# Kernel optimization log

Measured on AMD Instinct MI355X. Metric: run time of the kernel, lower is better.

## Reference

```python
import jax, jax.numpy as jnp
import numpy as np

S1, S2, B, H, E, IN, OUT, NL = 8, 32, 256, 1024, 512, 2, 2, 4


def setup_inputs() -> dict:
    key = jax.random.key(0)
    ks = jax.random.split(key, 20)
    s_h = 1.0 / np.sqrt(H)
    inp = {
        'input': jax.random.normal(ks[0], (B, IN), jnp.float32),
        'h0': jax.random.normal(ks[1], (NL, B, H), jnp.float32) * 0.5,
        'c0': jax.random.normal(ks[2], (NL, B, H), jnp.float32) * 0.5,
        'all_outputs': jax.random.normal(ks[3], (S1, S2, B, H), jnp.float32),
        'W_emb': jax.random.normal(ks[4], (E, IN), jnp.float32) / np.sqrt(IN),
        'b_emb': jax.random.normal(ks[5], (E,), jnp.float32) * 0.01,
        'W_attn': jax.random.normal(ks[6], (1, 2 * H), jnp.float32) / np.sqrt(2 * H),
        'b_attn': jax.random.normal(ks[7], (1,), jnp.float32) * 0.01,
        'Wih0': jax.random.normal(ks[8], (4 * H, E + H), jnp.float32) / np.sqrt(E + H),
        'Whh0': jax.random.normal(ks[9], (4 * H, H), jnp.float32) * s_h,
        'bih0': jax.random.normal(ks[10], (4 * H,), jnp.float32) * 0.01,
        'bhh0': jax.random.normal(ks[11], (4 * H,), jnp.float32) * 0.01,
        'Wih_r': jax.random.normal(ks[12], (NL - 1, 4 * H, H), jnp.float32) * s_h,
        'Whh_r': jax.random.normal(ks[13], (NL - 1, 4 * H, H), jnp.float32) * s_h,
        'bih_r': jax.random.normal(ks[14], (NL - 1, 4 * H), jnp.float32) * 0.01,
        'bhh_r': jax.random.normal(ks[15], (NL - 1, 4 * H), jnp.float32) * 0.01,
        'W_out': jax.random.normal(ks[16], (OUT, H), jnp.float32) * s_h,
        'b_out': jax.random.normal(ks[17], (OUT,), jnp.float32) * 0.01,
    }
    return inp


def _lstm_cell(x, h, c, Wih, Whh, bih, bhh):
    g = x @ Wih.T + h @ Whh.T + bih + bhh  # [B, 4H], torch gate order i,f,g,o
    i, f, gg, o = jnp.split(g, 4, axis=1)
    c2 = jax.nn.sigmoid(f) * c + jax.nn.sigmoid(i) * jnp.tanh(gg)
    h2 = jax.nn.sigmoid(o) * jnp.tanh(c2)
    return h2, c2


def reference(input, h0, c0, all_outputs, W_emb, b_emb, W_attn, b_attn,
              Wih0, Whh0, bih0, bhh0, Wih_r, Whh_r, bih_r, bhh_r, W_out, b_out):
    s1, s2, b, h_dim = all_outputs.shape
    # embedding (dropout = identity in eval mode)
    embedded = jax.nn.relu(input @ W_emb.T + b_emb)  # [B, E]
    h_top = h0[0]  # [B, H]
    # attn(cat(h_top, y)) decomposed: h part is shared across all (j, i)
    w_h = W_attn[0, :h_dim]
    w_y = W_attn[0, h_dim:]
    scores = (jnp.einsum('jibh,h->jib', all_outputs, w_y)
              + (h_top @ w_h)[None, None, :] + b_attn[0])  # [S1, S2, B]
    # torch cats per-(j,i) [B,1] columns j-major -> [B, S1*S2]
    normalized = jax.nn.softmax(scores.reshape(s1 * s2, b).T, axis=1)  # [B, S1*S2]
    temp = normalized.reshape(b, s1, s2)
    # NOTE: original writes into an expand()-ed zero buffer, so every j-slice
    # aliases the same memory; after the loop all slices equal the last j's bmm
    # result and sum(0) multiplies it by S1. We replicate that exactly.
    applied_last = jnp.einsum('bi,ibh->bh', temp[:, -1, :], all_outputs[-1])  # [B, H]
    final_attn = s1 * applied_last
    x = jnp.concatenate([final_attn, embedded], axis=1)  # [B, H+E]
    hs, cs = [], []
    h, c = _lstm_cell(x, h0[0], c0[0], Wih0, Whh0, bih0, bhh0)
    hs.append(h); cs.append(c)
    for l in range(Wih_r.shape[0]):  # inter-layer dropout = identity in eval
        h, c = _lstm_cell(h, h0[l + 1], c0[l + 1], Wih_r[l], Whh_r[l], bih_r[l], bhh_r[l])
        hs.append(h); cs.append(c)
    h_new = jnp.stack(hs)
    c_new = jnp.stack(cs)
    final_output = h @ W_out.T + b_out  # [B, OUT]
    return final_output, h_new, c_new, normalized
```

## Files before the change

### kernel.cpp

```cpp
#include <hip/hip_runtime.h>
#include <hip/hip_bf16.h>

typedef __bf16 bf16x8 __attribute__((ext_vector_type(8)));
typedef __bf16 bf16x4 __attribute__((ext_vector_type(4)));
typedef float  f32x4  __attribute__((ext_vector_type(4)));

#define KX 1536
#define G4 4096

#define O_FINAL 0
#define O_H     512
#define O_C     1049088
#define O_NORM  2097664

template<int K>
__device__ __forceinline__ void tile_gemm(const __bf16* __restrict__ A,
                                          const float* __restrict__ W,
                                          int r0, int j0,
                                          __bf16* __restrict__ At,
                                          __bf16* __restrict__ Wt,
                                          f32x4 acc[2]) {
  const int t = threadIdx.x;
  const int lane = t & 63, wave = t >> 6;
  const int rf = wave & 3, gg = wave >> 2;
  const int tr = t >> 3, chunk = t & 7;
  const int wrow = (tr >> 4) * 1024 + j0 + (tr & 15);
  const float*  wsrc = W + (size_t)wrow * K + chunk * 8;
  const __bf16* asrc = A + (size_t)(r0 + tr) * K + chunk * 8;
  const int sw_off = (chunk ^ (tr & 7)) << 4;
  char* wdst = (char*)Wt + tr * 128 + sw_off;
  char* adst = (char*)At + tr * 128 + sw_off;
  const int a_tr  = rf * 16 + (lane & 15);
  const int w_tr0 = gg * 32 + (lane & 15);
  const int w_tr1 = w_tr0 + 16;
  const int ksel  = lane >> 4;

  float4 wreg0 = *(const float4*)wsrc;
  float4 wreg1 = *(const float4*)(wsrc + 4);
  bf16x8 areg  = *(const bf16x8*)asrc;

  constexpr int NK = K / 64;
#pragma unroll 2
  for (int step = 0; step < NK; ++step) {
    __syncthreads();
    bf16x8 wv;
    wv[0] = (__bf16)wreg0.x; wv[1] = (__bf16)wreg0.y;
    wv[2] = (__bf16)wreg0.z; wv[3] = (__bf16)wreg0.w;
    wv[4] = (__bf16)wreg1.x; wv[5] = (__bf16)wreg1.y;
    wv[6] = (__bf16)wreg1.z; wv[7] = (__bf16)wreg1.w;
    *(bf16x8*)wdst = wv;
    *(bf16x8*)adst = areg;
    __syncthreads();
    if (step + 1 < NK) {
      wreg0 = *(const float4*)(wsrc + (step + 1) * 64);
      wreg1 = *(const float4*)(wsrc + (step + 1) * 64 + 4);
      areg  = *(const bf16x8*)(asrc + (step + 1) * 64);
    }
#pragma unroll
    for (int s = 0; s < 2; ++s) {
      const int chk = s * 4 + ksel;
      bf16x8 af  = *(const bf16x8*)((char*)At + a_tr  * 128 + ((chk ^ (a_tr  & 7)) << 4));
      bf16x8 wf0 = *(const bf16x8*)((char*)Wt + w_tr0 * 128 + ((chk ^ (w_tr0 & 7)) << 4));
      bf16x8 wf1 = *(const bf16x8*)((char*)Wt + w_tr1 * 128 + ((chk ^ (w_tr1 & 7)) << 4));
      acc[0] = __builtin_amdgcn_mfma_f32_16x16x32_bf16(af, wf0, acc[0], 0, 0, 0);
      acc[1] = __builtin_amdgcn_mfma_f32_16x16x32_bf16(af, wf1, acc[1], 0, 0, 0);
    }
  }
}

__global__ __launch_bounds__(256) void k_pre(const float* __restrict__ AO,
                                             const float* __restrict__ Wattn,
                                             const float* __restrict__ h0,
                                             float* __restrict__ sc,
                                             __bf16* __restrict__ h0b) {
  if (blockIdx.x >= 4096) {
    const int base = ((int)blockIdx.x - 4096) * 256 + threadIdx.x;
#pragma unroll
    for (int i = 0; i < 4; ++i) {
      int idx = base + i * 65536;
      float4 v = ((const float4*)h0)[idx];
      bf16x4 o;
      o[0] = (__bf16)v.x; o[1] = (__bf16)v.y; o[2] = (__bf16)v.z; o[3] = (__bf16)v.w;
      ((bf16x4*)h0b)[idx] = o;
    }
    return;
  }
  const int lane = threadIdx.x & 63, wave = threadIdx.x >> 6;
  const float* wy = Wattn + 1024;
  float4 wv[4];
#pragma unroll
  for (int q = 0; q < 4; ++q) wv[q] = *(const float4*)(wy + lane * 4 + 256 * q);
  const int row0 = (blockIdx.x * 4 + wave) * 4;
  float acc[4];
#pragma unroll
  for (int rr = 0; rr < 4; ++rr) {
    const float4* rp = (const float4*)(AO + (size_t)(row0 + rr) * 1024);
    float a = 0.f;
#pragma unroll
    for (int q = 0; q < 4; ++q) {
      float4 v = rp[lane + 64 * q];
      a += v.x * wv[q].x + v.y * wv[q].y + v.z * wv[q].z + v.w * wv[q].w;
    }
    acc[rr] = a;
  }
#pragma unroll
  for (int rr = 0; rr < 4; ++rr) {
    float a = acc[rr];
#pragma unroll
    for (int off = 32; off; off >>= 1) a += __shfl_xor(a, off, 64);
    if (lane == 0) {
      int row = row0 + rr;
      sc[(row & 255) * 256 + (row >> 8)] = a;
    }
  }
}

__global__ __launch_bounds__(512) void k_gh(const __bf16* __restrict__ h0b,
                                            const float* __restrict__ Whh0,
                                            const float* __restrict__ Whh_r,
                                            const float* __restrict__ bih0,
                                            const float* __restrict__ bhh0,
                                            const float* __restrict__ bih_r,
                                            const float* __restrict__ bhh_r,
                                            float* __restrict__ Gh) {
  __shared__ __bf16 At[64 * 64];
  __shared__ __bf16 Wt[64 * 64];
  const int l = blockIdx.x >> 8, inner = blockIdx.x & 255;
  const int cb = inner & 63, rb = inner >> 6;
  const int j0 = cb * 16, r0 = rb * 64;
  const __bf16* A = h0b + (size_t)l * 262144;
  const float* W  = (l == 0) ? Whh0 : (Whh_r + (size_t)(l - 1) * 4194304);
  const float* bi = (l == 0) ? bih0 : (bih_r + (size_t)(l - 1) * 4096);
  const float* bh = (l == 0) ? bhh0 : (bhh_r + (size_t)(l - 1) * 4096);
  f32x4 acc[2] = {};
  tile_gemm<1024>(A, W, r0, j0, At, Wt, acc);
  float* Go = Gh + (size_t)l * 1048576;
  const int lane = threadIdx.x & 63, wave = threadIdx.x >> 6;
  const int rf = wave & 3, gg = wave >> 2;
  const int col = j0 + (lane & 15);
  const int rbase = r0 + rf * 16 + ((lane >> 4) << 2);
#pragma unroll
  for (int gi = 0; gi < 2; ++gi) {
    const int cg = (gg * 2 + gi) * 1024 + col;
#pragma unroll
    for (int q = 0; q < 4; ++q)
      Go[(size_t)(rbase + q) * G4 + cg] = acc[gi][q] + bi[cg] + bh[cg];
  }
}

__global__ __launch_bounds__(256) void k_smx(const float* __restrict__ sc,
                                             const float* __restrict__ AO,
                                             const float* __restrict__ inp,
                                             const float* __restrict__ Wemb,
                                             const float* __restrict__ bemb,
                                             float* __restrict__ norm_out,
                                             __bf16* __restrict__ x) {
  __shared__ float red[4];
  __shared__ float wsm[32];
  const int b = blockIdx.x, t = threadIdx.x, lane = t & 63, wave = t >> 6;
  float s = sc[b * 256 + t];
  float m = s;
#pragma unroll
  for (int off = 32; off; off >>= 1) m = fmaxf(m, __shfl_xor(m, off, 64));
  if (lane == 0) red[wave] = m;
  __syncthreads();
  m = fmaxf(fmaxf(red[0], red[1]), fmaxf(red[2], red[3]));
  float e = __expf(s - m);
  float sum = e;
#pragma unroll
  for (int off = 32; off; off >>= 1) sum += __shfl_xor(sum, off, 64);
  __syncthreads();
  if (lane == 0) red[wave] = sum;
  __syncthreads();
  sum = red[0] + red[1] + red[2] + red[3];
  float nv = e / sum;
  norm_out[b * 256 + t] = nv;
  if (t >= 224) wsm[t - 224] = nv;
  __syncthreads();
  float acc[4] = {0.f, 0.f, 0.f, 0.f};
  const float* base = AO + ((size_t)224 * 256 + b) * 1024;
#pragma unroll 4
  for (int i = 0; i < 32; ++i) {
    float w = wsm[i];
    const float* rp = base + (size_t)i * 256 * 1024;
#pragma unroll
    for (int q = 0; q < 4; ++q) acc[q] += w * rp[t + 256 * q];
  }
#pragma unroll
  for (int q = 0; q < 4; ++q) x[(size_t)b * KX + t + 256 * q] = (__bf16)(8.0f * acc[q]);
  float i0 = inp[b * 2], i1 = inp[b * 2 + 1];
#pragma unroll
  for (int r = 0; r < 2; ++r) {
    int j = t + 256 * r;
    float e2 = i0 * Wemb[j * 2] + i1 * Wemb[j * 2 + 1] + bemb[j];
    x[(size_t)b * KX + 1024 + j] = (__bf16)fmaxf(e2, 0.f);
  }
}

template<int K>
__global__ __launch_bounds__(512) void k_layer(const __bf16* __restrict__ A,
                                               const float* __restrict__ Wih,
                                               const float* __restrict__ Gh,
                                               const float* __restrict__ c0,
                                               float* __restrict__ h_out,
                                               float* __restrict__ c_out,
                                               __bf16* __restrict__ hb) {
  __shared__ __bf16 At[64 * 64];
  __shared__ __bf16 Wt[64 * 64];
  __shared__ float exch[4][2][256];
  const int t = threadIdx.x, lane = t & 63, wave = t >> 6;
  const int rf = wave & 3, gg = wave >> 2;
  const int cb = blockIdx.x & 63, rb = blockIdx.x >> 6;
  const int j0 = cb * 16, r0 = rb * 64;
  f32x4 acc[2] = {};
  tile_gemm<K>(A, Wih, r0, j0, At, Wt, acc);
  const int col = j0 + (lane & 15);
  const int rbase = r0 + rf * 16 + ((lane >> 4) << 2);
#pragma unroll
  for (int gi = 0; gi < 2; ++gi) {
    const float* gp = Gh + (size_t)rbase * G4 + (gg * 2 + gi) * 1024 + col;
#pragma unroll
    for (int q = 0; q < 4; ++q) acc[gi][q] += gp[(size_t)q * G4];
  }
  const int eidx = ((lane >> 4) << 2) * 16 + (lane & 15);
  if (gg == 1) {
#pragma unroll
    for (int gi = 0; gi < 2; ++gi)
#pragma unroll
      for (int q = 0; q < 4; ++q)
        exch[rf][gi][eidx + q * 16] = acc[gi][q];
  }
  __syncthreads();
  if (gg == 0) {
#pragma unroll
    for (int q = 0; q < 4; ++q) {
      const int b = rbase + q;
      float gv = exch[rf][0][eidx + q * 16];
      float ov = exch[rf][1][eidx + q * 16];
      float si = 1.f / (1.f + __expf(-acc[0][q]));
      float sf = 1.f / (1.f + __expf(-acc[1][q]));
      float so = 1.f / (1.f + __expf(-ov));
      float c2 = sf * c0[(size_t)b * 1024 + col] + si * tanhf(gv);
      float h2 = so * tanhf(c2);
      h_out[(size_t)b * 1024 + col] = h2;
      c_out[(size_t)b * 1024 + col] = c2;
      hb[(size_t)b * 1024 + col] = (__bf16)h2;
    }
  }
}

__global__ __launch_bounds__(256) void k_final(const float* __restrict__ h3,
                                               const float* __restrict__ Wout,
                                               const float* __restrict__ bout,
                                               float* __restrict__ out) {
  const int lane = threadIdx.x & 63, wave = threadIdx.x >> 6;
  const int b = blockIdx.x * 4 + wave;
  const float4* hp = (const float4*)(h3 + (size_t)b * 1024);
  const float4* w0 = (const float4*)Wout;
  const float4* w1 = (const float4*)(Wout + 1024);
  float a0 = 0.f, a1 = 0.f;
#pragma unroll
  for (int q = 0; q < 4; ++q) {
    float4 hv = hp[lane + 64 * q];
    float4 v0 = w0[lane + 64 * q];
    float4 v1 = w1[lane + 64 * q];
    a0 += hv.x * v0.x + hv.y * v0.y + hv.z * v0.z + hv.w * v0.w;
    a1 += hv.x * v1.x + hv.y * v1.y + hv.z * v1.z + hv.w * v1.w;
  }
#pragma unroll
  for (int off = 32; off; off >>= 1) {
    a0 += __shfl_xor(a0, off, 64);
    a1 += __shfl_xor(a1, off, 64);
  }
  if (lane == 0) {
    out[b * 2]     = a0 + bout[0];
    out[b * 2 + 1] = a1 + bout[1];
  }
}

extern "C" void kernel_launch(void* const* d_in, const int* in_sizes, int n_in,
                              void* d_out, int out_size, void* d_ws, size_t ws_size,
                              hipStream_t stream) {
  const float* inp    = (const float*)d_in[0];
  const float* h0     = (const float*)d_in[1];
  const float* c0     = (const float*)d_in[2];
  const float* AO     = (const float*)d_in[3];
  const float* Wemb   = (const float*)d_in[4];
  const float* bemb   = (const float*)d_in[5];
  const float* Wattn  = (const float*)d_in[6];
  const float* Wih0   = (const float*)d_in[8];
  const float* Whh0   = (const float*)d_in[9];
  const float* bih0   = (const float*)d_in[10];
  const float* bhh0   = (const float*)d_in[11];
  const float* Wih_r  = (const float*)d_in[12];
  const float* Whh_r  = (const float*)d_in[13];
  const float* bih_r  = (const float*)d_in[14];
  const float* bhh_r  = (const float*)d_in[15];
  const float* Wout   = (const float*)d_in[16];
  const float* bout   = (const float*)d_in[17];

  float* out = (float*)d_out;
  char* ws = (char*)d_ws;

  float*  sc  = (float*)(ws + 0);
  float*  Gh  = (float*)(ws + (1u << 18));
  __bf16* xb  = (__bf16*)(ws + 17039360);
  __bf16* h0b = (__bf16*)(ws + 17825792);
  __bf16* hb  = (__bf16*)(ws + 19922944);

  k_pre<<<4352, 256, 0, stream>>>(AO, Wattn, h0, sc, h0b);
  k_gh<<<1024, 512, 0, stream>>>(h0b, Whh0, Whh_r, bih0, bhh0, bih_r, bhh_r, Gh);
  k_smx<<<256, 256, 0, stream>>>(sc, AO, inp, Wemb, bemb, out + O_NORM, xb);

  for (int l = 0; l < 4; ++l) {
    const __bf16* A1 = (l == 0) ? xb : (hb + (size_t)(l - 1) * 262144);
    float* h_out = out + O_H + (size_t)l * 262144;
    float* c_out = out + O_C + (size_t)l * 262144;
    if (l == 0)
      k_layer<1536><<<256, 512, 0, stream>>>(A1, Wih0, Gh, c0, h_out, c_out, hb);
    else
      k_layer<1024><<<256, 512, 0, stream>>>(A1, Wih_r + (size_t)(l - 1) * 4194304,
                                             Gh + (size_t)l * 1048576,
                                             c0 + (size_t)l * 262144,
                                             h_out, c_out,
                                             hb + (size_t)l * 262144);
  }

  k_final<<<64, 256, 0, stream>>>(out + O_H + 3 * 262144, Wout, bout, out + O_FINAL);
}
```

Baseline: 181.2 us.

## Fuse front kernels and precast input-gate weights to bf16 for layer GEMMs

Merges the attention-score, hidden-gate GEMM and a new weight-conversion pass into one wide front kernel. That kernel converts all Wih matrices to bf16 in parallel, so the four serial layer kernels stream half as many weight bytes. The Whh GEMM now reads fp32 h0 directly instead of a separate bf16 copy. The trade is extra total memory traffic (a bf16 weight write plus a reread) in exchange for a shorter serial critical path and one fewer launch.

```diff
diff --git a/kernel.cpp b/kernel.cpp
--- a/kernel.cpp
+++ b/kernel.cpp
@@ -4,28 +4,78 @@
 typedef __bf16 bf16x8 __attribute__((ext_vector_type(8)));
 typedef __bf16 bf16x4 __attribute__((ext_vector_type(4)));
 typedef float  f32x4  __attribute__((ext_vector_type(4)));
-
-#define KX 1536
-#define G4 4096
 
 #define O_FINAL 0
 #define O_H     512
 #define O_C     1049088
 #define O_NORM  2097664
 
+__device__ __forceinline__ bf16x8 cvt8(float4 a, float4 b) {
+  bf16x8 r;
+  r[0] = (__bf16)a.x; r[1] = (__bf16)a.y; r[2] = (__bf16)a.z; r[3] = (__bf16)a.w;
+  r[4] = (__bf16)b.x; r[5] = (__bf16)b.y; r[6] = (__bf16)b.z; r[7] = (__bf16)b.w;
+  return r;
+}
+
 template<int K>
-__device__ __forceinline__ void tile_gemm(const __bf16* __restrict__ A,
-                                          const float* __restrict__ W,
-                                          int r0, int j0,
-                                          __bf16* __restrict__ At,
-                                          __bf16* __restrict__ Wt,
-                                          f32x4 acc[2]) {
-  const int t = threadIdx.x;
-  const int lane = t & 63, wave = t >> 6;
+__device__ __forceinline__ void tile_gemm_ff(const float* __restrict__ A,
+                                             const float* __restrict__ W,
+                                             int r0, int j0,
+                                             __bf16* __restrict__ At,
+                                             __bf16* __restrict__ Wt,
+                                             f32x4 acc[2]) {
+  const int t = threadIdx.x, lane = t & 63, wave = t >> 6;
   const int rf = wave & 3, gg = wave >> 2;
   const int tr = t >> 3, chunk = t & 7;
-  const int wrow = (tr >> 4) * 1024 + j0 + (tr & 15);
-  const float*  wsrc = W + (size_t)wrow * K + chunk * 8;
+  const float* wsrc = W + (size_t)((tr >> 4) * 1024 + j0 + (tr & 15)) * K + chunk * 8;
+  const float* asrc = A + (size_t)(r0 + tr) * K + chunk * 8;
+  const int sw_off = (chunk ^ (tr & 7)) << 4;
+  char* wdst = (char*)Wt + tr * 128 + sw_off;
+  char* adst = (char*)At + tr * 128 + sw_off;
+  const int a_tr  = rf * 16 + (lane & 15);
+  const int w_tr0 = gg * 32 + (lane & 15);
+  const int w_tr1 = w_tr0 + 16;
+  const int ksel  = lane >> 4;
+
+  float4 wr0 = *(const float4*)wsrc, wr1 = *(const float4*)(wsrc + 4);
+  float4 ar0 = *(const float4*)asrc, ar1 = *(const float4*)(asrc + 4);
+
+  constexpr int NK = K / 64;
+#pragma unroll 2
+  for (int step = 0; step < NK; ++step) {
+    __syncthreads();
+    *(bf16x8*)wdst = cvt8(wr0, wr1);
+    *(bf16x8*)adst = cvt8(ar0, ar1);
+    __syncthreads();
+    if (step + 1 < NK) {
+      wr0 = *(const float4*)(wsrc + (step + 1) * 64);
+      wr1 = *(const float4*)(wsrc + (step + 1) * 64 + 4);
+      ar0 = *(const float4*)(asrc + (step + 1) * 64);
+      ar1 = *(const float4*)(asrc + (step + 1) * 64 + 4);
+    }
+#pragma unroll
+    for (int s = 0; s < 2; ++s) {
+      const int chk = s * 4 + ksel;
+      bf16x8 af  = *(const bf16x8*)((char*)At + a_tr  * 128 + ((chk ^ (a_tr  & 7)) << 4));
+      bf16x8 wf0 = *(const bf16x8*)((char*)Wt + w_tr0 * 128 + ((chk ^ (w_tr0 & 7)) << 4));
+      bf16x8 wf1 = *(const bf16x8*)((char*)Wt + w_tr1 * 128 + ((chk ^ (w_tr1 & 7)) << 4));
+      acc[0] = __builtin_amdgcn_mfma_f32_16x16x32_bf16(af, wf0, acc[0], 0, 0, 0);
+      acc[1] = __builtin_amdgcn_mfma_f32_16x16x32_bf16(af, wf1, acc[1], 0, 0, 0);
+    }
+  }
+}
+
+template<int K>
+__device__ __forceinline__ void tile_gemm_bb(const __bf16* __restrict__ A,
+                                             const __bf16* __restrict__ W,
+                                             int r0, int j0,
+                                             __bf16* __restrict__ At,
+                                             __bf16* __restrict__ Wt,
+                                             f32x4 acc[2]) {
+  const int t = threadIdx.x, lane = t & 63, wave = t >> 6;
+  const int rf = wave & 3, gg = wave >> 2;
+  const int tr = t >> 3, chunk = t & 7;
+  const __bf16* wsrc = W + (size_t)((tr >> 4) * 1024 + j0 + (tr & 15)) * K + chunk * 8;
   const __bf16* asrc = A + (size_t)(r0 + tr) * K + chunk * 8;
   const int sw_off = (chunk ^ (tr & 7)) << 4;
   char* wdst = (char*)Wt + tr * 128 + sw_off;
@@ -35,26 +85,19 @@
   const int w_tr1 = w_tr0 + 16;
   const int ksel  = lane >> 4;
 
-  float4 wreg0 = *(const float4*)wsrc;
-  float4 wreg1 = *(const float4*)(wsrc + 4);
-  bf16x8 areg  = *(const bf16x8*)asrc;
+  bf16x8 wr = *(const bf16x8*)wsrc;
+  bf16x8 ar = *(const bf16x8*)asrc;
 
   constexpr int NK = K / 64;
 #pragma unroll 2
   for (int step = 0; step < NK; ++step) {
     __syncthreads();
-    bf16x8 wv;
-    wv[0] = (__bf16)wreg0.x; wv[1] = (__bf16)wreg0.y;
-    wv[2] = (__bf16)wreg0.z; wv[3] = (__bf16)wreg0.w;
-    wv[4] = (__bf16)wreg1.x; wv[5] = (__bf16)wreg1.y;
-    wv[6] = (__bf16)wreg1.z; wv[7] = (__bf16)wreg1.w;
-    *(bf16x8*)wdst = wv;
-    *(bf16x8*)adst = areg;
+    *(bf16x8*)wdst = wr;
+    *(bf16x8*)adst = ar;
     __syncthreads();
     if (step + 1 < NK) {
-      wreg0 = *(const float4*)(wsrc + (step + 1) * 64);
-      wreg1 = *(const float4*)(wsrc + (step + 1) * 64 + 4);
-      areg  = *(const bf16x8*)(asrc + (step + 1) * 64);
+      wr = *(const bf16x8*)(wsrc + (step + 1) * 64);
+      ar = *(const bf16x8*)(asrc + (step + 1) * 64);
     }
 #pragma unroll
     for (int s = 0; s < 2; ++s) {
@@ -68,83 +111,82 @@
   }
 }
 
-__global__ __launch_bounds__(256) void k_pre(const float* __restrict__ AO,
-                                             const float* __restrict__ Wattn,
-                                             const float* __restrict__ h0,
-                                             float* __restrict__ sc,
-                                             __bf16* __restrict__ h0b) {
-  if (blockIdx.x >= 4096) {
-    const int base = ((int)blockIdx.x - 4096) * 256 + threadIdx.x;
-#pragma unroll
-    for (int i = 0; i < 4; ++i) {
-      int idx = base + i * 65536;
-      float4 v = ((const float4*)h0)[idx];
-      bf16x4 o;
-      o[0] = (__bf16)v.x; o[1] = (__bf16)v.y; o[2] = (__bf16)v.z; o[3] = (__bf16)v.w;
-      ((bf16x4*)h0b)[idx] = o;
+__global__ __launch_bounds__(512) void k_front(
+    const float* __restrict__ AO, const float* __restrict__ Wattn,
+    float* __restrict__ sc,
+    const float* __restrict__ h0,
+    const float* __restrict__ Whh0, const float* __restrict__ Whh_r,
+    const float* __restrict__ bih0, const float* __restrict__ bhh0,
+    const float* __restrict__ bih_r, const float* __restrict__ bhh_r,
+    float* __restrict__ Gh,
+    const float* __restrict__ Wih0, const float* __restrict__ Wih_r,
+    __bf16* __restrict__ Wihb) {
+  const int t = threadIdx.x, lane = t & 63, wave = t >> 6;
+  if (blockIdx.x < 2048) {
+    const float* wy = Wattn + 1024;
+    float4 wv[4];
+#pragma unroll
+    for (int q = 0; q < 4; ++q) wv[q] = *(const float4*)(wy + lane * 4 + 256 * q);
+    const int row0 = (blockIdx.x * 8 + wave) * 4;
+    float a4[4];
+#pragma unroll
+    for (int rr = 0; rr < 4; ++rr) {
+      const float4* rp = (const float4*)(AO + (size_t)(row0 + rr) * 1024);
+      float a = 0.f;
+#pragma unroll
+      for (int q = 0; q < 4; ++q) {
+        float4 v = rp[lane + 64 * q];
+        a += v.x * wv[q].x + v.y * wv[q].y + v.z * wv[q].z + v.w * wv[q].w;
+      }
+      a4[rr] = a;
+    }
+#pragma unroll
+    for (int rr = 0; rr < 4; ++rr) {
+      float a = a4[rr];
+#pragma unroll
+      for (int off = 32; off; off >>= 1) a += __shfl_xor(a, off, 64);
+      if (lane == 0) {
+        int row = row0 + rr;
+        sc[(row & 255) * 256 + (row >> 8)] = a;
+      }
     }
     return;
   }
-  const int lane = threadIdx.x & 63, wave = threadIdx.x >> 6;
-  const float* wy = Wattn + 1024;
-  float4 wv[4];
-#pragma unroll
-  for (int q = 0; q < 4; ++q) wv[q] = *(const float4*)(wy + lane * 4 + 256 * q);
-  const int row0 = (blockIdx.x * 4 + wave) * 4;
-  float acc[4];
-#pragma unroll
-  for (int rr = 0; rr < 4; ++rr) {
-    const float4* rp = (const float4*)(AO + (size_t)(row0 + rr) * 1024);
-    float a = 0.f;
-#pragma unroll
-    for (int q = 0; q < 4; ++q) {
-      float4 v = rp[lane + 64 * q];
-      a += v.x * wv[q].x + v.y * wv[q].y + v.z * wv[q].z + v.w * wv[q].w;
-    }
-    acc[rr] = a;
-  }
-#pragma unroll
-  for (int rr = 0; rr < 4; ++rr) {
-    float a = acc[rr];
-#pragma unroll
-    for (int off = 32; off; off >>= 1) a += __shfl_xor(a, off, 64);
-    if (lane == 0) {
-      int row = row0 + rr;
-      sc[(row & 255) * 256 + (row >> 8)] = a;
-    }
-  }
-}
-
-__global__ __launch_bounds__(512) void k_gh(const __bf16* __restrict__ h0b,
-                                            const float* __restrict__ Whh0,
-                                            const float* __restrict__ Whh_r,
-                                            const float* __restrict__ bih0,
-                                            const float* __restrict__ bhh0,
-                                            const float* __restrict__ bih_r,
-                                            const float* __restrict__ bhh_r,
-                                            float* __restrict__ Gh) {
-  __shared__ __bf16 At[64 * 64];
-  __shared__ __bf16 Wt[64 * 64];
-  const int l = blockIdx.x >> 8, inner = blockIdx.x & 255;
-  const int cb = inner & 63, rb = inner >> 6;
-  const int j0 = cb * 16, r0 = rb * 64;
-  const __bf16* A = h0b + (size_t)l * 262144;
-  const float* W  = (l == 0) ? Whh0 : (Whh_r + (size_t)(l - 1) * 4194304);
-  const float* bi = (l == 0) ? bih0 : (bih_r + (size_t)(l - 1) * 4096);
-  const float* bh = (l == 0) ? bhh0 : (bhh_r + (size_t)(l - 1) * 4096);
-  f32x4 acc[2] = {};
-  tile_gemm<1024>(A, W, r0, j0, At, Wt, acc);
-  float* Go = Gh + (size_t)l * 1048576;
-  const int lane = threadIdx.x & 63, wave = threadIdx.x >> 6;
-  const int rf = wave & 3, gg = wave >> 2;
-  const int col = j0 + (lane & 15);
-  const int rbase = r0 + rf * 16 + ((lane >> 4) << 2);
-#pragma unroll
-  for (int gi = 0; gi < 2; ++gi) {
-    const int cg = (gg * 2 + gi) * 1024 + col;
-#pragma unroll
-    for (int q = 0; q < 4; ++q)
-      Go[(size_t)(rbase + q) * G4 + cg] = acc[gi][q] + bi[cg] + bh[cg];
+  if (blockIdx.x < 3072) {
+    __shared__ __bf16 At[64 * 64];
+    __shared__ __bf16 Wt[64 * 64];
+    const int j = blockIdx.x - 2048;
+    const int l = j >> 8, inner = j & 255;
+    const int cb = inner & 63, rb = inner >> 6;
+    const int j0 = cb * 16, r0 = rb * 64;
+    const float* A  = h0 + (size_t)l * 262144;
+    const float* W  = (l == 0) ? Whh0 : (Whh_r + (size_t)(l - 1) * 4194304);
+    const float* bi = (l == 0) ? bih0 : (bih_r + (size_t)(l - 1) * 4096);
+    const float* bh = (l == 0) ? bhh0 : (bhh_r + (size_t)(l - 1) * 4096);
+    f32x4 acc[2] = {};
+    tile_gemm_ff<1024>(A, W, r0, j0, At, Wt, acc);
+    float* Go = Gh + (size_t)l * 1048576;
+    const int rf = wave & 3, gg = wave >> 2;
+    const int col = j0 + (lane & 15);
+    const int rbase = r0 + rf * 16 + ((lane >> 4) << 2);
+#pragma unroll
+    for (int gi = 0; gi < 2; ++gi) {
+      const int cg = (gg * 2 + gi) * 1024 + col;
+#pragma unroll
+      for (int q = 0; q < 4; ++q)
+        Go[(size_t)(rbase + q) * 4096 + cg] = acc[gi][q] + bi[cg] + bh[cg];
+    }
+    return;
+  }
+  const int tid = ((int)blockIdx.x - 3072) * 512 + t;
+#pragma unroll
+  for (int n = 0; n < 8; ++n) {
+    int idx = tid + n * 589824;
+    float4 v = (idx < 1572864) ? ((const float4*)Wih0)[idx]
+                               : ((const float4*)Wih_r)[idx - 1572864];
+    bf16x4 o;
+    o[0] = (__bf16)v.x; o[1] = (__bf16)v.y; o[2] = (__bf16)v.z; o[3] = (__bf16)v.w;
+    ((bf16x4*)Wihb)[idx] = o;
   }
 }
 
@@ -182,26 +224,26 @@
 #pragma unroll 4
   for (int i = 0; i < 32; ++i) {
     float w = wsm[i];
-    const float* rp = base + (size_t)i * 256 * 1024;
+    const float* rp = base + (size_t)i * 262144;
 #pragma unroll
     for (int q = 0; q < 4; ++q) acc[q] += w * rp[t + 256 * q];
   }
 #pragma unroll
-  for (int q = 0; q < 4; ++q) x[(size_t)b * KX + t + 256 * q] = (__bf16)(8.0f * acc[q]);
+  for (int q = 0; q < 4; ++q) x[(size_t)b * 1536 + t + 256 * q] = (__bf16)(8.0f * acc[q]);
   float i0 = inp[b * 2], i1 = inp[b * 2 + 1];
 #pragma unroll
   for (int r = 0; r < 2; ++r) {
-    int j = t + 256 * r;
-    float e2 = i0 * Wemb[j * 2] + i1 * Wemb[j * 2 + 1] + bemb[j];
-    x[(size_t)b * KX + 1024 + j] = (__bf16)fmaxf(e2, 0.f);
+    int jj = t + 256 * r;
+    float e2 = i0 * Wemb[jj * 2] + i1 * Wemb[jj * 2 + 1] + bemb[jj];
+    x[(size_t)b * 1536 + 1024 + jj] = (__bf16)fmaxf(e2, 0.f);
   }
 }
 
 template<int K>
 __global__ __launch_bounds__(512) void k_layer(const __bf16* __restrict__ A,
-                                               const float* __restrict__ Wih,
+                                               const __bf16* __restrict__ Wb,
                                                const float* __restrict__ Gh,
-                                               const float* __restrict__ c0,
+                                               const float* __restrict__ c0l,
                                                float* __restrict__ h_out,
                                                float* __restrict__ c_out,
                                                __bf16* __restrict__ hb) {
@@ -213,14 +255,14 @@
   const int cb = blockIdx.x & 63, rb = blockIdx.x >> 6;
   const int j0 = cb * 16, r0 = rb * 64;
   f32x4 acc[2] = {};
-  tile_gemm<K>(A, Wih, r0, j0, At, Wt, acc);
+  tile_gemm_bb<K>(A, Wb, r0, j0, At, Wt, acc);
   const int col = j0 + (lane & 15);
   const int rbase = r0 + rf * 16 + ((lane >> 4) << 2);
 #pragma unroll
   for (int gi = 0; gi < 2; ++gi) {
-    const float* gp = Gh + (size_t)rbase * G4 + (gg * 2 + gi) * 1024 + col;
-#pragma unroll
-    for (int q = 0; q < 4; ++q) acc[gi][q] += gp[(size_t)q * G4];
+    const float* gp = Gh + (size_t)rbase * 4096 + (gg * 2 + gi) * 1024 + col;
+#pragma unroll
+    for (int q = 0; q < 4; ++q) acc[gi][q] += gp[(size_t)q * 4096];
   }
   const int eidx = ((lane >> 4) << 2) * 16 + (lane & 15);
   if (gg == 1) {
@@ -234,17 +276,17 @@
   if (gg == 0) {
 #pragma unroll
     for (int q = 0; q < 4; ++q) {
-      const int b = rbase + q;
+      const int row = rbase + q;
       float gv = exch[rf][0][eidx + q * 16];
       float ov = exch[rf][1][eidx + q * 16];
       float si = 1.f / (1.f + __expf(-acc[0][q]));
       float sf = 1.f / (1.f + __expf(-acc[1][q]));
       float so = 1.f / (1.f + __expf(-ov));
-      float c2 = sf * c0[(size_t)b * 1024 + col] + si * tanhf(gv);
+      float c2 = sf * c0l[(size_t)row * 1024 + col] + si * tanhf(gv);
       float h2 = so * tanhf(c2);
-      h_out[(size_t)b * 1024 + col] = h2;
-      c_out[(size_t)b * 1024 + col] = c2;
-      hb[(size_t)b * 1024 + col] = (__bf16)h2;
+      h_out[(size_t)row * 1024 + col] = h2;
+      c_out[(size_t)row * 1024 + col] = c2;
+      hb[(size_t)row * 1024 + col] = (__bf16)h2;
     }
   }
 }
@@ -302,29 +344,29 @@
   float* out = (float*)d_out;
   char* ws = (char*)d_ws;
 
-  float*  sc  = (float*)(ws + 0);
-  float*  Gh  = (float*)(ws + (1u << 18));
-  __bf16* xb  = (__bf16*)(ws + 17039360);
-  __bf16* h0b = (__bf16*)(ws + 17825792);
-  __bf16* hb  = (__bf16*)(ws + 19922944);
-
-  k_pre<<<4352, 256, 0, stream>>>(AO, Wattn, h0, sc, h0b);
-  k_gh<<<1024, 512, 0, stream>>>(h0b, Whh0, Whh_r, bih0, bhh0, bih_r, bhh_r, Gh);
+  __bf16* Wihb  = (__bf16*)ws;
+  float*  Gh    = (float*)(ws + 37748736);
+  __bf16* xb    = (__bf16*)(ws + 54525952);
+  __bf16* hb    = (__bf16*)(ws + 55312384);
+  float*  sc    = (float*)(ws + 57409536);
+  __bf16* Wihb0 = Wihb;
+  __bf16* Wihbr = Wihb + 6291456;
+
+  k_front<<<4224, 512, 0, stream>>>(AO, Wattn, sc, h0, Whh0, Whh_r,
+                                    bih0, bhh0, bih_r, bhh_r, Gh,
+                                    Wih0, Wih_r, Wihb);
   k_smx<<<256, 256, 0, stream>>>(sc, AO, inp, Wemb, bemb, out + O_NORM, xb);
 
-  for (int l = 0; l < 4; ++l) {
-    const __bf16* A1 = (l == 0) ? xb : (hb + (size_t)(l - 1) * 262144);
-    float* h_out = out + O_H + (size_t)l * 262144;
-    float* c_out = out + O_C + (size_t)l * 262144;
-    if (l == 0)
-      k_layer<1536><<<256, 512, 0, stream>>>(A1, Wih0, Gh, c0, h_out, c_out, hb);
-    else
-      k_layer<1024><<<256, 512, 0, stream>>>(A1, Wih_r + (size_t)(l - 1) * 4194304,
-                                             Gh + (size_t)l * 1048576,
-                                             c0 + (size_t)l * 262144,
-                                             h_out, c_out,
-                                             hb + (size_t)l * 262144);
-  }
+  k_layer<1536><<<256, 512, 0, stream>>>(xb, Wihb0, Gh, c0,
+                                         out + O_H, out + O_C, hb);
+  for (int l = 1; l < 4; ++l)
+    k_layer<1024><<<256, 512, 0, stream>>>(hb + (size_t)(l - 1) * 262144,
+                                           Wihbr + (size_t)(l - 1) * 4194304,
+                                           Gh + (size_t)l * 1048576,
+                                           c0 + (size_t)l * 262144,
+                                           out + O_H + (size_t)l * 262144,
+                                           out + O_C + (size_t)l * 262144,
+                                           hb + (size_t)l * 262144);
 
   k_final<<<64, 256, 0, stream>>>(out + O_H + 3 * 262144, Wout, bout, out + O_FINAL);
 }
```

Result: faster. 166.3 us (-8.2%).
